# Kernel tuning notes

Hardware: AMD Instinct MI355X
Metric: run time of the kernel (lower is better)

## Reference

```python
import jax, jax.numpy as jnp
import numpy as np

# --- module configuration (mirrors init_kwargs) ---
B = 32
ROWS, COLS = 8, 8
M = ROWS * COLS              # num_macs
CMS, NEUR = 8, 16            # num_cms_per_mac, num_neurons_per_cm
P_ROWS, P_COLS = 12, 12
PM = P_ROWS * P_COLS         # prev_layer_num_macs
P_CMS, P_NEUR = 8, 16
PF = P_CMS * P_NEUR          # prev-layer features per MAC
RF_RADIUS = 0.5              # mac_receptive_field_size
SIG_PHI, SIG_LAM, SIG_CHI = 0.5, 28.0, 2.5
MIN_FAM = 0.2
ACT_MIN, ACT_MAX = 0.2, 1.0


def _mac_positions(num, rows, cols, layout='rect'):
    off = 0.5 if layout == 'hex' else 0.0
    col_sp = 0.0
    row_loc = [0.5] if rows == 1 else [i / (rows - 1) for i in range(rows)]
    if cols == 1:
        col_loc = [0.5]
    else:
        col_sp = 1.0 / (cols - 1)
        col_loc = [i * col_sp for i in range(cols)]
    return [(row_loc[i // cols], col_loc[i % cols] + off * ((i % rows) % 2) * col_sp)
            for i in range(num)]


def _connections():
    """Replicates find_connected_macs_in_prev_layer: per-MAC list of prev-layer
    MAC indices within RF_RADIUS, padded with PM (the zero row)."""
    cur = _mac_positions(M, ROWS, COLS)
    prev = _mac_positions(PM, P_ROWS, P_COLS)
    conns, sizes = [], []
    for (r, c) in cur:
        idx = [j for j, (pr, pc) in enumerate(prev)
               if ((r - pr) ** 2 + (c - pc) ** 2) ** 0.5 <= RF_RADIUS]
        conns.append(idx)
        sizes.append(len(idx))
    mx = max(len(c) for c in conns)
    conns = [c + [PM] * (mx - len(c)) for c in conns]
    return np.asarray(conns, np.int32), np.asarray(sizes, np.float32)


def setup_inputs() -> dict:
    key = jax.random.key(0)
    k1, k2 = jax.random.split(key, 2)
    conns, rf_sizes = _connections()
    R = conns.shape[1]
    # Sparsey input code: one active neuron per CM of each prev-layer MAC.
    winners = jax.random.randint(k1, (B, PM, P_CMS), 0, P_NEUR)
    x = jax.nn.one_hot(winners, P_NEUR, dtype=jnp.float32).reshape(B, PM, PF)
    # Weights are Hebbian-learned in [0,1]; random here for a non-trivial baseline.
    weights = jax.random.uniform(k2, (M, R * PF, CMS * NEUR), dtype=jnp.float32)
    thr_min = jnp.asarray((rf_sizes * (ACT_MIN * P_CMS))[None, :, None])
    thr_max = jnp.asarray((rf_sizes * (ACT_MAX * P_CMS))[None, :, None])
    return {"x": x, "weights": weights,
            "input_connections": jnp.asarray(conns),
            "thr_min": thr_min, "thr_max": thr_max}


def reference(x, weights, input_connections, thr_min, thr_max):
    b = x.shape[0]
    # pad with a zero MAC so padded connection index PM gathers zeros
    xp = jnp.concatenate([x, jnp.zeros((b, 1, x.shape[2]), x.dtype)], axis=1)
    g = xp[:, input_connections]                 # (B, M, R, PF) gather
    g = g.reshape(b, M, -1)                      # (B, M, R*PF)
    sums = g.sum(axis=-1, keepdims=True)         # (B, M, 1)
    active = ((sums >= thr_min) & (sums <= thr_max)).astype(x.dtype)
    raw = jnp.einsum('bmi,mio->bmo', g, weights)  # per-MAC batched matmul
    h = (raw / jnp.maximum(sums, 1.0)).reshape(b, M, CMS, NEUR)  # normalized input sums
    fam = h.max(axis=-1).mean(axis=-1)           # familiarity G: (B, M)
    eta = SIG_CHI / (1.0 + jnp.exp(-SIG_LAM * (fam - SIG_PHI)))
    eta = jnp.where(fam >= MIN_FAM, eta, 0.0)    # below min familiarity -> uniform dist
    probs = jax.nn.softmax(eta[:, :, None, None] * h, axis=-1)  # (B, M, CMS, NEUR)
    # Categorical sampling per CM via Gumbel-max with a fixed key
    gmb = jax.random.gumbel(jax.random.key(42), probs.shape, dtype=probs.dtype)
    winners = jnp.argmax(jnp.log(probs + 1e-30) + gmb, axis=-1)  # (B, M, CMS)
    out = jax.nn.one_hot(winners, NEUR, dtype=x.dtype) * active[..., None]
    return out.reshape(b, M, CMS * NEUR)
```

## Files before the change

### kernel.cpp

```cpp
#include <hip/hip_runtime.h>
#include <stdint.h>

#define NB 32
#define NM 64
#define NPM 144
#define NPF 128
#define NCMS 8
#define NNEUR 16
#define NOUT 128
#define RMAX 256
#define NC 16

__device__ __forceinline__ uint32_t rotl32(uint32_t x, int d) {
  return (x << d) | (x >> (32 - d));
}

__device__ __forceinline__ void threefry2x32(uint32_t& x0, uint32_t& x1) {
  const uint32_t k0 = 0u, k1 = 42u;
  const uint32_t k2 = 0x1BD11BDAu ^ k0 ^ k1;
  x0 += k0; x1 += k1;
#define TF_R(r) { x0 += x1; x1 = rotl32(x1, (r)); x1 ^= x0; }
  TF_R(13) TF_R(15) TF_R(26) TF_R(6)  x0 += k1; x1 += k2 + 1u;
  TF_R(17) TF_R(29) TF_R(16) TF_R(24) x0 += k2; x1 += k0 + 2u;
  TF_R(13) TF_R(15) TF_R(26) TF_R(6)  x0 += k0; x1 += k1 + 3u;
  TF_R(17) TF_R(29) TF_R(16) TF_R(24) x0 += k1; x1 += k2 + 4u;
  TF_R(13) TF_R(15) TF_R(26) TF_R(6)  x0 += k2; x1 += k0 + 5u;
#undef TF_R
}

__device__ __forceinline__ float gumbel_at(uint32_t idx) {
  uint32_t x0 = 0u, x1 = idx;
  threefry2x32(x0, x1);
  uint32_t bits = x0 ^ x1;
  float f = __uint_as_float((bits >> 9) | 0x3f800000u) - 1.0f;
  float u = fmaxf(f, 1.17549435e-38f);
  return -logf(-logf(u));
}

__global__ __launch_bounds__(128) void k_winners(const float* __restrict__ x,
                                                 unsigned char* __restrict__ win) {
  const int pm = blockIdx.x;
  const int b0 = blockIdx.y * 8;
  const int tid = threadIdx.x;
  const int grp = tid >> 4, lane16 = tid & 15;
#pragma unroll
  for (int i = 0; i < 8; ++i) {
    int b = b0 + i;
    float xv = x[((size_t)b * NPM + pm) * NPF + tid];
    unsigned long long msk = __ballot(xv > 0.5f);
    int base = (tid & 63) & ~15;
    int wv = __builtin_ctzll((msk >> base) & 0xFFFFull);
    if (lane16 == 0) win[pm * 256 + grp * 32 + b] = (unsigned char)wv;
  }
}

__global__ __launch_bounds__(256) void k_gather(
    const float* __restrict__ w, const int* __restrict__ conns,
    const unsigned char* __restrict__ win, float* __restrict__ part, int R) {
  const int bid = blockIdx.x;
  const int m = (bid * 21) & 63;
  const int c = bid >> 6;
  const int tid = threadIdx.x;
  const int oq = tid & 31;
  const int bg = tid >> 5;

  __shared__ int s_conn[32];
  __shared__ unsigned char s_winb[16 * 256];

  int nv = 0;
  for (int base = 0; base < R; base += 256) {
    int r = base + tid;
    int pmv = (r < R) ? conns[m * R + r] : NPM;
    nv += __syncthreads_count(pmv != NPM);
  }
  const int s = (nv * c) / NC, e = (nv * (c + 1)) / NC;
  const int clen = e - s;

  if (tid < clen) s_conn[tid] = conns[m * R + s + tid];
  __syncthreads();
  for (int idx = tid; idx < clen * 256; idx += 256) {
    int rr = idx >> 8;
    s_winb[idx] = win[s_conn[rr] * 256 + (idx & 255)];
  }
  __syncthreads();

  const float* wm = w + (size_t)m * ((size_t)R * NPF * NOUT);

  float facc[4][4] = {};
  double dacc[4][4] = {};

  const int n = clen * 8;
  for (int it = 0; it < n; ++it) {
    const int rr = it >> 3, cm = it & 7;
    const uint32_t w4 =
        *(const uint32_t*)&s_winb[(rr << 8) + (cm << 5) + (bg << 2)];
    const float* wp = wm + (((size_t)(s + rr) * NPF + (cm << 4)) << 7);
#pragma unroll
    for (int bb = 0; bb < 4; ++bb) {
      int row = (w4 >> (bb * 8)) & 15;
      const float4 v = *(const float4*)(wp + (row << 7) + (oq << 2));
      facc[bb][0] += v.x; facc[bb][1] += v.y;
      facc[bb][2] += v.z; facc[bb][3] += v.w;
    }
    if ((it & 7) == 7) {
#pragma unroll
      for (int bb = 0; bb < 4; ++bb) {
#pragma unroll
        for (int k = 0; k < 4; ++k) {
          dacc[bb][k] += (double)facc[bb][k];
          facc[bb][k] = 0.0f;
        }
      }
    }
  }

  float* pb = part + ((size_t)c * NM + m) * NB * NOUT;
#pragma unroll
  for (int bb = 0; bb < 4; ++bb) {
    float4 v;
    v.x = (float)dacc[bb][0]; v.y = (float)dacc[bb][1];
    v.z = (float)dacc[bb][2]; v.w = (float)dacc[bb][3];
    *(float4*)(pb + (size_t)(bg * 4 + bb) * NOUT + (oq << 2)) = v;
  }
}

__global__ __launch_bounds__(128) void k_epilogue(
    const float* __restrict__ part, const int* __restrict__ conns,
    const float* __restrict__ thr_min, const float* __restrict__ thr_max,
    float* __restrict__ out, int R) {
  const int tid = threadIdx.x;
  const int m = blockIdx.x >> 5, b = blockIdx.x & 31;
  const int grp = tid >> 4, lane16 = tid & 15;
  __shared__ float s_red[8];

  int nv = 0;
  for (int base = 0; base < R; base += 128) {
    int r = base + tid;
    int pmv = (r < R) ? conns[m * R + r] : NPM;
    nv += __syncthreads_count(pmv != NPM);
  }

  double acc = 0.0;
#pragma unroll
  for (int c = 0; c < NC; ++c)
    acc += (double)part[(((size_t)c * NM + m) * NB + b) * NOUT + tid];

  float sums = 8.0f * (float)nv;
  float h = (float)acc / fmaxf(sums, 1.0f);

  float hm = h;
#pragma unroll
  for (int off = 8; off >= 1; off >>= 1) hm = fmaxf(hm, __shfl_xor(hm, off, 16));
  if (lane16 == 0) s_red[grp] = hm;
  __syncthreads();
  float fam = s_red[0];
#pragma unroll
  for (int cc = 1; cc < 8; ++cc) fam += s_red[cc];
  fam *= 0.125f;

  float eta = 2.5f / (1.0f + expf(-28.0f * (fam - 0.5f)));
  if (!(fam >= 0.2f)) eta = 0.0f;

  float v = eta * h;
  float vm = v;
#pragma unroll
  for (int off = 8; off >= 1; off >>= 1) vm = fmaxf(vm, __shfl_xor(vm, off, 16));
  float ee = expf(v - vm);
  float ss = ee;
#pragma unroll
  for (int off = 8; off >= 1; off >>= 1) ss += __shfl_xor(ss, off, 16);
  float p = ee / ss;

  uint32_t idx = (uint32_t)(((b * NM + m) * NCMS + grp) * NNEUR + lane16);
  float y = logf(p + 1e-30f) + gumbel_at(idx);

  float bv = y;
  int bi = lane16;
#pragma unroll
  for (int off = 8; off >= 1; off >>= 1) {
    float ov = __shfl_xor(bv, off, 16);
    int oi = __shfl_xor(bi, off, 16);
    if (ov > bv || (ov == bv && oi < bi)) { bv = ov; bi = oi; }
  }

  float act = (sums >= thr_min[m] && sums <= thr_max[m]) ? 1.0f : 0.0f;
  out[(size_t)(b * NM + m) * NOUT + tid] = (lane16 == bi) ? act : 0.0f;
}

__global__ __launch_bounds__(128) void sparsey_fallback(
    const float* __restrict__ x, const float* __restrict__ w,
    const int* __restrict__ conns, const float* __restrict__ thr_min,
    const float* __restrict__ thr_max, float* __restrict__ out, int R) {
  const int tid = threadIdx.x;
  const int bid = blockIdx.x;
  const int m = bid >> 5;
  const int b = bid & 31;

  __shared__ int s_conn[RMAX];
  __shared__ unsigned char s_win[RMAX * 8];
  __shared__ float s_red[8];

  for (int r = tid; r < R; r += 128) s_conn[r] = conns[m * R + r];
  __syncthreads();

  const int grp = tid >> 4;
  const int lane16 = tid & 15;

  int nvalid = 0;
  const float* xb = x + (size_t)b * (NPM * NPF);
  for (int r = 0; r < R; ++r) {
    int pm = s_conn[r];
    if (pm == NPM) continue;
    ++nvalid;
    float xv = xb[(size_t)pm * NPF + tid];
    unsigned long long msk = __ballot(xv > 0.5f);
    int base = (tid & 63) & ~15;
    int wv = __builtin_ctzll((msk >> base) & 0xFFFFull);
    if (lane16 == 0) s_win[r * 8 + grp] = (unsigned char)wv;
  }
  __syncthreads();

  double acc = 0.0;
  const float* wm = w + (size_t)m * ((size_t)R * NPF * NOUT);
  for (int r = 0; r < R; ++r) {
    if (s_conn[r] == NPM) continue;
    const float* wr = wm + (size_t)r * (NPF * NOUT);
#pragma unroll
    for (int cm = 0; cm < 8; ++cm) {
      int row = cm * 16 + (int)s_win[r * 8 + cm];
      acc += (double)wr[row * NOUT + tid];
    }
  }

  float sums = 8.0f * (float)nvalid;
  float h = (float)acc / fmaxf(sums, 1.0f);

  float hm = h;
#pragma unroll
  for (int off = 8; off >= 1; off >>= 1) hm = fmaxf(hm, __shfl_xor(hm, off, 16));
  if (lane16 == 0) s_red[grp] = hm;
  __syncthreads();
  float fam = s_red[0];
#pragma unroll
  for (int c = 1; c < 8; ++c) fam += s_red[c];
  fam *= 0.125f;

  float eta = 2.5f / (1.0f + expf(-28.0f * (fam - 0.5f)));
  if (!(fam >= 0.2f)) eta = 0.0f;

  float v = eta * h;
  float vm = v;
#pragma unroll
  for (int off = 8; off >= 1; off >>= 1) vm = fmaxf(vm, __shfl_xor(vm, off, 16));
  float e = expf(v - vm);
  float ssum = e;
#pragma unroll
  for (int off = 8; off >= 1; off >>= 1) ssum += __shfl_xor(ssum, off, 16);
  float p = e / ssum;

  uint32_t idx = (uint32_t)(((b * NM + m) * NCMS + grp) * NNEUR + lane16);
  float y = logf(p + 1e-30f) + gumbel_at(idx);

  float bv = y;
  int bi = lane16;
#pragma unroll
  for (int off = 8; off >= 1; off >>= 1) {
    float ov = __shfl_xor(bv, off, 16);
    int oi = __shfl_xor(bi, off, 16);
    if (ov > bv || (ov == bv && oi < bi)) { bv = ov; bi = oi; }
  }

  float act = (sums >= thr_min[m] && sums <= thr_max[m]) ? 1.0f : 0.0f;
  out[(size_t)(b * NM + m) * NOUT + tid] = (lane16 == bi) ? act : 0.0f;
}

extern "C" void kernel_launch(void* const* d_in, const int* in_sizes, int n_in,
                              void* d_out, int out_size, void* d_ws, size_t ws_size,
                              hipStream_t stream) {
  const float* x = (const float*)d_in[0];
  const float* w = (const float*)d_in[1];
  const int* conns = (const int*)d_in[2];
  const float* tmin = (const float*)d_in[3];
  const float* tmax = (const float*)d_in[4];
  float* out = (float*)d_out;

  const int R = in_sizes[2] / NM;

  const size_t WIN_BYTES = 65536;
  const size_t PART_BYTES = (size_t)NC * NM * NB * NOUT * sizeof(float);

  if (ws_size < WIN_BYTES + PART_BYTES || R > RMAX) {
    sparsey_fallback<<<dim3(NM * NB), 128, 0, stream>>>(x, w, conns, tmin, tmax,
                                                        out, R);
    return;
  }

  unsigned char* win = (unsigned char*)d_ws;
  float* part = (float*)((char*)d_ws + WIN_BYTES);

  k_winners<<<dim3(NPM, 4), 128, 0, stream>>>(x, win);
  k_gather<<<dim3(NM * NC), 256, 0, stream>>>(w, conns, win, part, R);
  k_epilogue<<<dim3(NM * NB), 128, 0, stream>>>(part, conns, tmin, tmax, out, R);
}
```

Baseline: 63.12 us.

## Halve gather chunk count and unroll CM loop to batch weight loads

The number of receptive-field chunks per MAC drops from 16 to 8, so each block handles twice as many connections and fewer partial sums are written and reduced. The inner loop is restructured to walk connections with a fully unrolled per-CM loop that issues eight float4 gathers before accumulating, raising memory-level parallelism. Shared buffers grow to 32 connections, and a new fallback guard rejects larger R. The risk is fewer blocks in flight (512 instead of 1024) and higher register pressure.

```diff
diff --git a/kernel.cpp b/kernel.cpp
--- a/kernel.cpp
+++ b/kernel.cpp
@@ -9,7 +9,8 @@
 #define NNEUR 16
 #define NOUT 128
 #define RMAX 256
-#define NC 16
+#define NC 8
+#define CLEN_MAX 32
 
 __device__ __forceinline__ uint32_t rotl32(uint32_t x, int d) {
   return (x << d) | (x >> (32 - d));
@@ -61,11 +62,11 @@
   const int m = (bid * 21) & 63;
   const int c = bid >> 6;
   const int tid = threadIdx.x;
-  const int oq = tid & 31;
+  const int oq4 = (tid & 31) << 2;
   const int bg = tid >> 5;
 
-  __shared__ int s_conn[32];
-  __shared__ unsigned char s_winb[16 * 256];
+  __shared__ int s_conn[CLEN_MAX];
+  __shared__ unsigned char s_winb[CLEN_MAX * 256];
 
   int nv = 0;
   for (int base = 0; base < R; base += 256) {
@@ -84,32 +85,46 @@
   }
   __syncthreads();
 
-  const float* wm = w + (size_t)m * ((size_t)R * NPF * NOUT);
+  const float* wbase =
+      w + (size_t)m * ((size_t)R * NPF * NOUT) + ((size_t)s << 14);
 
   float facc[4][4] = {};
   double dacc[4][4] = {};
 
-  const int n = clen * 8;
-  for (int it = 0; it < n; ++it) {
-    const int rr = it >> 3, cm = it & 7;
-    const uint32_t w4 =
-        *(const uint32_t*)&s_winb[(rr << 8) + (cm << 5) + (bg << 2)];
-    const float* wp = wm + (((size_t)(s + rr) * NPF + (cm << 4)) << 7);
+  for (int rr = 0; rr < clen; ++rr) {
+    const float* wr = wbase + ((size_t)rr << 14);
+    const uint32_t* wrow = (const uint32_t*)&s_winb[rr << 8];
+#pragma unroll
+    for (int cm = 0; cm < 8; cm += 2) {
+      const uint32_t w4a = wrow[(cm << 3) + bg];
+      const uint32_t w4b = wrow[((cm + 1) << 3) + bg];
+      const float* wca = wr + (cm << 11);
+      const float* wcb = wca + (1 << 11);
+      float4 va[4], vb[4];
+#pragma unroll
+      for (int bb = 0; bb < 4; ++bb) {
+        int row = (w4a >> (bb * 8)) & 15;
+        va[bb] = *(const float4*)(wca + (row << 7) + oq4);
+      }
+#pragma unroll
+      for (int bb = 0; bb < 4; ++bb) {
+        int row = (w4b >> (bb * 8)) & 15;
+        vb[bb] = *(const float4*)(wcb + (row << 7) + oq4);
+      }
+#pragma unroll
+      for (int bb = 0; bb < 4; ++bb) {
+        facc[bb][0] += va[bb].x; facc[bb][1] += va[bb].y;
+        facc[bb][2] += va[bb].z; facc[bb][3] += va[bb].w;
+        facc[bb][0] += vb[bb].x; facc[bb][1] += vb[bb].y;
+        facc[bb][2] += vb[bb].z; facc[bb][3] += vb[bb].w;
+      }
+    }
 #pragma unroll
     for (int bb = 0; bb < 4; ++bb) {
-      int row = (w4 >> (bb * 8)) & 15;
-      const float4 v = *(const float4*)(wp + (row << 7) + (oq << 2));
-      facc[bb][0] += v.x; facc[bb][1] += v.y;
-      facc[bb][2] += v.z; facc[bb][3] += v.w;
-    }
-    if ((it & 7) == 7) {
-#pragma unroll
-      for (int bb = 0; bb < 4; ++bb) {
-#pragma unroll
-        for (int k = 0; k < 4; ++k) {
-          dacc[bb][k] += (double)facc[bb][k];
-          facc[bb][k] = 0.0f;
-        }
+#pragma unroll
+      for (int k = 0; k < 4; ++k) {
+        dacc[bb][k] += (double)facc[bb][k];
+        facc[bb][k] = 0.0f;
       }
     }
   }
@@ -120,7 +135,7 @@
     float4 v;
     v.x = (float)dacc[bb][0]; v.y = (float)dacc[bb][1];
     v.z = (float)dacc[bb][2]; v.w = (float)dacc[bb][3];
-    *(float4*)(pb + (size_t)(bg * 4 + bb) * NOUT + (oq << 2)) = v;
+    *(float4*)(pb + (size_t)((bg << 2) + bb) * NOUT + oq4) = v;
   }
 }
 
@@ -289,7 +304,7 @@
   const size_t WIN_BYTES = 65536;
   const size_t PART_BYTES = (size_t)NC * NM * NB * NOUT * sizeof(float);
 
-  if (ws_size < WIN_BYTES + PART_BYTES || R > RMAX) {
+  if (ws_size < WIN_BYTES + PART_BYTES || R > RMAX || R > CLEN_MAX * NC) {
     sparsey_fallback<<<dim3(NM * NB), 128, 0, stream>>>(x, w, conns, tmin, tmax,
                                                         out, R);
     return;
```

New measurement: 94.14 us. 49.1% more time.
